# Performance work log

Hardware: AMD Instinct MI355X
Metric: run time of the kernel (lower is better)

## Reference

```python
import jax, jax.numpy as jnp
import numpy as np

B, T, D, H, K, V = 2, 2048, 2048, 16, 128, 128


def _l2norm(x, eps=1e-12):
    # F.normalize(p=2, dim=-1)
    n = jnp.sqrt(jnp.sum(x * x, axis=-1, keepdims=True))
    return x / jnp.maximum(n, eps)


def setup_inputs() -> dict:
    key = jax.random.key(0)
    ks = jax.random.split(key, 7)
    s = D ** -0.5
    return {
        "x": jax.random.normal(ks[0], (B, T, D), jnp.float32),
        "Wq": jax.random.normal(ks[1], (H * K, D), jnp.float32) * s,
        "Wk": jax.random.normal(ks[2], (H * K, D), jnp.float32) * s,
        "Wv": jax.random.normal(ks[3], (H * V, D), jnp.float32) * s,
        "Wa": jax.random.normal(ks[4], (H, D), jnp.float32) * s,
        "ba": jnp.zeros((H,), jnp.float32),
        "Wb": jax.random.normal(ks[5], (H, D), jnp.float32) * s,
        "bb": jnp.zeros((H,), jnp.float32),
    }


def _forward(x, Wq, Wk, Wv, Wa, ba, Wb, bb):
    Bq, Tq, _ = x.shape
    # projections (nn.Linear: y = x @ W.T)
    q = _l2norm(jnp.einsum('btd,od->bto', x, Wq).reshape(Bq, Tq, H, K))
    k = _l2norm(jnp.einsum('btd,od->bto', x, Wk).reshape(Bq, Tq, H, K))
    v = jnp.einsum('btd,od->bto', x, Wv).reshape(Bq, Tq, H, V)
    alpha = jax.nn.sigmoid(jnp.einsum('btd,hd->bth', x, Wa) + ba)          # [B,T,H] decay in (0,1)
    beta = jax.nn.softplus(jnp.einsum('btd,hd->bth', x, Wb) + bb) * K ** (-0.5)

    # gated delta rule recurrence over time (vectorized over B,H):
    #   S_t = a_t * S_{t-1} (I - b_t k_t k_t^T) + b_t v_t k_t^T ;  o_t = S_t q_t
    def step(S, inp):
        q_t, k_t, v_t, a_t, b_t = inp  # [B,H,K],[B,H,K],[B,H,V],[B,H],[B,H]
        Sd = S * a_t[..., None, None]                              # decay  [B,H,V,K]
        pred = jnp.einsum('bhvk,bhk->bhv', Sd, k_t)                # S k
        u = b_t[..., None] * (v_t - pred)                          # delta update [B,H,V]
        S_new = Sd + u[..., None] * k_t[:, :, None, :]             # rank-1 write
        o_t = jnp.einsum('bhvk,bhk->bhv', S_new, q_t)
        return S_new, o_t

    S0 = jnp.zeros((Bq, H, V, K), x.dtype)
    xs = (q.transpose(1, 0, 2, 3), k.transpose(1, 0, 2, 3),
          v.transpose(1, 0, 2, 3), alpha.transpose(1, 0, 2), beta.transpose(1, 0, 2))
    _, o = jax.lax.scan(step, S0, xs)
    return o.transpose(1, 0, 2, 3)  # [B,T,H,V]


def reference(x, Wq, Wk, Wv, Wa, ba, Wb, bb):
    return _forward(x, Wq, Wk, Wv, Wa, ba, Wb, bb)
```

## Files before the change

kernel.cpp:

```cpp
#include <hip/hip_runtime.h>
#include <math.h>

#define BB 2
#define TT 2048
#define DD 2048
#define HH 16
#define KK 128

typedef _Float16 h4 __attribute__((ext_vector_type(4)));
typedef _Float16 v8h __attribute__((ext_vector_type(8)));
typedef float v4f __attribute__((ext_vector_type(4)));
typedef float f2 __attribute__((ext_vector_type(2)));
typedef unsigned int u2v __attribute__((ext_vector_type(2)));

__global__ __launch_bounds__(256) void gemm_nt3(const float* __restrict__ A,
                                                const float* __restrict__ W0,
                                                const float* __restrict__ W1,
                                                const float* __restrict__ W2,
                                                float* __restrict__ Cbase,
                                                int M, int N, int Kd) {
  __shared__ float As[8][128];
  __shared__ float Bs[8][128];
  const int z = blockIdx.z;
  const float* W = (z == 0) ? W0 : (z == 1) ? W1 : W2;
  float* C = Cbase + (size_t)z * M * N;
  const int tid = threadIdx.x;
  const int bm = blockIdx.y * 128;
  const int bn = blockIdx.x * 128;
  const int lrow = tid >> 1;
  const int lcol = (tid & 1) * 4;
  const int rm = (tid >> 4) * 8;
  const int rn = (tid & 15) * 8;
  const float* Ap = A + (size_t)(bm + lrow) * Kd + lcol;
  const float* Wp = W + (size_t)(bn + lrow) * Kd + lcol;
  float acc[8][8];
#pragma unroll
  for (int i = 0; i < 8; i++)
#pragma unroll
    for (int j = 0; j < 8; j++) acc[i][j] = 0.f;
  float4 av = *(const float4*)Ap;
  float4 wv = *(const float4*)Wp;
  for (int d0 = 0; d0 < Kd; d0 += 8) {
    __syncthreads();
    As[lcol + 0][lrow] = av.x; As[lcol + 1][lrow] = av.y;
    As[lcol + 2][lrow] = av.z; As[lcol + 3][lrow] = av.w;
    Bs[lcol + 0][lrow] = wv.x; Bs[lcol + 1][lrow] = wv.y;
    Bs[lcol + 2][lrow] = wv.z; Bs[lcol + 3][lrow] = wv.w;
    __syncthreads();
    if (d0 + 8 < Kd) {
      av = *(const float4*)(Ap + d0 + 8);
      wv = *(const float4*)(Wp + d0 + 8);
    }
#pragma unroll
    for (int kk = 0; kk < 8; kk++) {
      const float4 a0 = *(const float4*)&As[kk][rm];
      const float4 a1 = *(const float4*)&As[kk][rm + 4];
      const float4 b0 = *(const float4*)&Bs[kk][rn];
      const float4 b1 = *(const float4*)&Bs[kk][rn + 4];
      const float ar[8] = {a0.x, a0.y, a0.z, a0.w, a1.x, a1.y, a1.z, a1.w};
      const float br[8] = {b0.x, b0.y, b0.z, b0.w, b1.x, b1.y, b1.z, b1.w};
#pragma unroll
      for (int i = 0; i < 8; i++)
#pragma unroll
        for (int j = 0; j < 8; j++) acc[i][j] = fmaf(ar[i], br[j], acc[i][j]);
    }
  }
#pragma unroll
  for (int i = 0; i < 8; i++) {
    float* cp = C + (size_t)(bm + rm + i) * N + bn + rn;
    float4 c0 = {acc[i][0], acc[i][1], acc[i][2], acc[i][3]};
    float4 c1 = {acc[i][4], acc[i][5], acc[i][6], acc[i][7]};
    *(float4*)cp = c0;
    *(float4*)(cp + 4) = c1;
  }
}

__global__ __launch_bounds__(256) void convert_f16(
    const float* __restrict__ x, const float* __restrict__ Wq,
    const float* __restrict__ Wk, const float* __restrict__ Wv,
    _Float16* __restrict__ xh, _Float16* __restrict__ Wf) {
  const size_t N4X = (size_t)BB * TT * DD / 4;
  const size_t N4W = (size_t)(HH * KK) * DD / 4;
  const size_t i = (size_t)blockIdx.x * 256 + threadIdx.x;
  if (i < N4X) {
    const float4 v = ((const float4*)x)[i];
    h4 hi;
    hi.x = (_Float16)v.x; hi.y = (_Float16)v.y;
    hi.z = (_Float16)v.z; hi.w = (_Float16)v.w;
    ((h4*)xh)[i] = hi;
  } else {
    const size_t j = i - N4X;
    const float* Ws = (j < N4W) ? Wq : (j < 2 * N4W) ? Wk : Wv;
    const size_t jj = (j < N4W) ? j : (j < 2 * N4W) ? (j - N4W) : (j - 2 * N4W);
    const float4 v = ((const float4*)Ws)[jj];
    h4 hi;
    hi.x = (_Float16)v.x; hi.y = (_Float16)v.y;
    hi.z = (_Float16)v.z; hi.w = (_Float16)v.w;
    ((h4*)Wf)[j] = hi;
  }
}

#define GLDS(gp, lp)                                              \
  __builtin_amdgcn_global_load_lds(                               \
      (const __attribute__((address_space(1))) void*)(gp),        \
      (__attribute__((address_space(3))) void*)(lp), 16, 0, 0)

__global__ __launch_bounds__(256) void gemm_mfma(
    const _Float16* __restrict__ xh, const _Float16* __restrict__ Wf,
    float* __restrict__ Cbase) {
  __shared__ float4 lraw[1024];
  _Float16* Ah = (_Float16*)lraw;
  _Float16* Bs = Ah + 4096;

  const int z = blockIdx.z;
  const _Float16* W = Wf + (size_t)z * DD * (HH * KK);
  float* C = Cbase + (size_t)z * (BB * TT) * (HH * KK);

  const int tid = threadIdx.x;
  const int w = tid >> 6;
  const int lane = tid & 63;
  const int bm = blockIdx.y * 128;
  const int bn = blockIdx.x * 128;
  const int wm = (w & 1) * 64;
  const int wn = (w >> 1) * 64;
  const int m16 = lane & 15;
  const int quad = lane >> 4;

  const _Float16* gA = xh + (size_t)(bm + (tid >> 2)) * DD + (tid & 3) * 8;
  const _Float16* gB = W + (size_t)(bn + (tid >> 2)) * DD + (tid & 3) * 8;
  const int lb = w * 512;

  v4f acc[4][4];
#pragma unroll
  for (int i = 0; i < 4; i++)
#pragma unroll
    for (int j = 0; j < 4; j++) acc[i][j] = (v4f){0.f, 0.f, 0.f, 0.f};

  for (int d0 = 0; d0 < DD; d0 += 32) {
    GLDS(gA + d0, Ah + lb);
    GLDS(gA + d0 + 64 * DD, Ah + 2048 + lb);
    GLDS(gB + d0, Bs + lb);
    GLDS(gB + d0 + 64 * DD, Bs + 2048 + lb);
    __syncthreads();
    v8h ah[4], bw[4];
#pragma unroll
    for (int i = 0; i < 4; i++) {
      ah[i] = *(const v8h*)&Ah[(wm + i * 16 + m16) * 32 + quad * 8];
      bw[i] = *(const v8h*)&Bs[(wn + i * 16 + m16) * 32 + quad * 8];
    }
#pragma unroll
    for (int mi = 0; mi < 4; mi++)
#pragma unroll
      for (int ni = 0; ni < 4; ni++)
        acc[mi][ni] = __builtin_amdgcn_mfma_f32_16x16x32_f16(ah[mi], bw[ni],
                                                             acc[mi][ni], 0, 0, 0);
    __syncthreads();
  }
#pragma unroll
  for (int mi = 0; mi < 4; mi++) {
#pragma unroll
    for (int r = 0; r < 4; r++) {
      float* cp =
          C + (size_t)(bm + wm + mi * 16 + quad * 4 + r) * (HH * KK) + bn + wn + m16;
#pragma unroll
      for (int ni = 0; ni < 4; ni++) cp[ni * 16] = acc[mi][ni][r];
    }
  }
}

__global__ __launch_bounds__(256) void ab_proj(const float* __restrict__ x,
                                               const float* __restrict__ Wa,
                                               const float* __restrict__ ba,
                                               const float* __restrict__ Wb,
                                               const float* __restrict__ bb,
                                               float* __restrict__ abq) {
  const int row = blockIdx.x;
  const int g = threadIdx.x >> 6;
  const int lane = threadIdx.x & 63;
  const int h0 = (g & 1) * 8;
  const bool isA = (g < 2);
  const float* W = isA ? Wa : Wb;
  const float* xr = x + (size_t)row * DD;
  float acc[8];
#pragma unroll
  for (int j = 0; j < 8; j++) acc[j] = 0.f;
  for (int d = lane; d < DD; d += 64) {
    const float xv = xr[d];
#pragma unroll
    for (int j = 0; j < 8; j++)
      acc[j] = fmaf(xv, W[(size_t)(h0 + j) * DD + d], acc[j]);
  }
#pragma unroll
  for (int j = 0; j < 8; j++) {
#pragma unroll
    for (int off = 32; off > 0; off >>= 1) acc[j] += __shfl_xor(acc[j], off, 64);
  }
  if (lane == 0) {
    if (isA) {
#pragma unroll
      for (int j = 0; j < 8; j++) {
        const float z = acc[j] + ba[h0 + j];
        abq[((size_t)row * HH + h0 + j) * 4 + 0] = 1.0f / (1.0f + expf(-z));
      }
    } else {
#pragma unroll
      for (int j = 0; j < 8; j++) {
        const float z = acc[j] + bb[h0 + j];
        const float sp = (z > 20.f) ? z : log1pf(expf(z));
        abq[((size_t)row * HH + h0 + j) * 4 + 1] = sp * 0.08838834764831845f;
      }
    }
  }
}

__global__ __launch_bounds__(256) void norm_qk(float* __restrict__ q,
                                               float* __restrict__ k,
                                               float* __restrict__ abq) {
  const int vec = blockIdx.x * 4 + (threadIdx.x >> 6);
  const int l = threadIdx.x & 63;
  float* qp = q + (size_t)vec * 128;
  float* kp = k + (size_t)vec * 128;
  float q0 = qp[l], q1 = qp[l + 64];
  float k0 = kp[l], k1 = kp[l + 64];
  float sq = q0 * q0 + q1 * q1;
  float sk = k0 * k0 + k1 * k1;
#pragma unroll
  for (int off = 32; off > 0; off >>= 1) {
    sq += __shfl_xor(sq, off, 64);
    sk += __shfl_xor(sk, off, 64);
  }
  const float iq = 1.0f / fmaxf(sqrtf(sq), 1e-12f);
  const float ik = 1.0f / fmaxf(sqrtf(sk), 1e-12f);
  q0 *= iq; q1 *= iq; k0 *= ik; k1 *= ik;
  qp[l] = q0; qp[l + 64] = q1;
  kp[l] = k0; kp[l + 64] = k1;
  float pq = q0 * k0 + q1 * k1;
#pragma unroll
  for (int off = 32; off > 0; off >>= 1) pq += __shfl_xor(pq, off, 64);
  if (l == 0) {
    abq[(size_t)vec * 4 + 2] = pq;
    abq[(size_t)vec * 4 + 3] =
        abq[(size_t)vec * 4 + 0] * abq[(size_t)vec * 4 + 1];
  }
}

#define DPP_ADD(x, ctrl)                                                     \
  ((x) + __int_as_float(__builtin_amdgcn_update_dpp(                         \
             0, __float_as_int(x), (ctrl), 0xF, 0xF, true)))

__device__ __forceinline__ float xadd32(float x) {
  const u2v r = __builtin_amdgcn_permlane32_swap(__float_as_uint(x),
                                                 __float_as_uint(x), false,
                                                 false);
  return __uint_as_float(r.x) + __uint_as_float(r.y);
}

#define SBAR() asm volatile("s_barrier" ::: "memory")
#define WAITV(n) asm volatile("s_waitcnt vmcnt(" #n ")" ::: "memory")

#define SCAN_MATH(kc, qc, vc, ac, jj, obname)                                  \
  {                                                                            \
    const f2 ka = {kc.x, kc.y};                                                \
    const f2 kb2 = {kc.z, kc.w};                                               \
    const f2 qa = {qc.x, qc.y};                                                \
    const f2 qb2 = {qc.z, qc.w};                                               \
    const f2 pdk = __builtin_elementwise_fma(Sb, kb2, Sa * ka);                \
    const f2 pdq = __builtin_elementwise_fma(Sb, qb2, Sa * qa);                \
    float dk = pdk.x + pdk.y;                                                  \
    float dq = pdq.x + pdq.y;                                                  \
    dk = DPP_ADD(dk, 0xB1);  dq = DPP_ADD(dq, 0xB1);                           \
    dk = DPP_ADD(dk, 0x4E);  dq = DPP_ADD(dq, 0x4E);                           \
    dk = DPP_ADD(dk, 0x141); dq = DPP_ADD(dq, 0x141);                          \
    dk = DPP_ADD(dk, 0x140); dq = DPP_ADD(dq, 0x140);                          \
    dk = xadd32(dk);         dq = xadd32(dq);                                  \
    const float u = ac.y * fmaf(-ac.x, dk, vc);                                \
    const float oo = fmaf(ac.x, dq, u * ac.z);                                 \
    const f2 a2 = {ac.x, ac.x};                                                \
    const f2 u2 = {u, u};                                                      \
    Sa = __builtin_elementwise_fma(a2, Sa, u2 * ka);                           \
    Sb = __builtin_elementwise_fma(a2, Sb, u2 * kb2);                          \
    obname = (ks == (jj)) ? oo : obname;                                       \
  }

#define STAGE(bi, tg)                                                          \
  {                                                                            \
    const float* gk =                                                          \
        kU + (size_t)((tg) + 2 * w + (lane >> 5)) * 2048 + (lane & 31) * 4;    \
    GLDS(gk, &Kb[bi][2 * w][0]);                                               \
    const float* gq =                                                          \
        qU + (size_t)((tg) + 2 * w + (lane >> 5)) * 2048 + (lane & 31) * 4;    \
    GLDS(gq, &Qb[bi][2 * w][0]);                                               \
    if (lane < 8) GLDS(aU + (size_t)((tg) + lane) * 64, &Ab[bi][0][0]);        \
    _Pragma("unroll") for (int jj = 0; jj < 8; jj++)                           \
        vf##bi[jj] = vU[vrow + (size_t)((tg) + jj) * 2048];                    \
  }

#define COMPUTE_GROUP(bi, obname)                                              \
  float obname = 0.f;                                                          \
  _Pragma("unroll") for (int j = 0; j < 8; j++) {                              \
    const float4 kc = *(const float4*)&Kb[bi][j][ks4];                         \
    const float4 qc = *(const float4*)&Qb[bi][j][ks4];                         \
    const float4 ac = *(const float4*)&Ab[bi][j][0];                           \
    const float vc = vf##bi[j];                                                \
    SCAN_MATH(kc, qc, vc, ac, j, obname);                                      \
  }

__global__ __launch_bounds__(256, 2) void scan_kernel(
    const float* __restrict__ q, const float* __restrict__ k,
    const float* __restrict__ v, const float* __restrict__ abq,
    float* __restrict__ o) {
  __shared__ float Kb[2][8][128];
  __shared__ float Qb[2][8][128];
  __shared__ float Ab[2][8][4];

  const int bid = blockIdx.x;
  const int bh = bid & 31;
  const int s = bid >> 5;
  const int h = bh & 15;
  const int b = bh >> 4;
  const int tid = threadIdx.x;
  const int w = tid >> 6;
  const int lane = tid & 63;
  const int rg = (lane >> 4) & 1;
  const int ks = (lane & 15) | ((lane >> 5) << 4);
  const int ks4 = ks * 4;
  const int vrow = s * 8 + w * 2 + rg;

  const size_t base = (size_t)b * TT * 2048 + (size_t)h * KK;
  const float* kU = k + base;
  const float* qU = q + base;
  const float* vU = v + base;
  const float* aU = abq + ((size_t)b * TT * HH + h) * 4;
  float* oU = o + base;

  f2 Sa = {0.f, 0.f}, Sb = {0.f, 0.f};
  float vf0[8], vf1[8];

  STAGE(0, 0);
  STAGE(1, 8);
  WAITV(11);
  SBAR();
  __builtin_amdgcn_sched_barrier(0);

  int tg = 0;
  for (int gp = 0; gp < TT / 8; gp += 2) {
    COMPUTE_GROUP(0, ob0);
    if (ks < 8) oU[vrow + (size_t)(tg + ks) * 2048] = ob0;
    SBAR();
    if (gp + 2 < TT / 8) {
      STAGE(0, tg + 16);
      WAITV(11);
    } else {
      WAITV(0);
    }
    SBAR();
    __builtin_amdgcn_sched_barrier(0);

    COMPUTE_GROUP(1, ob1);
    if (ks < 8) oU[vrow + (size_t)(tg + 8 + ks) * 2048] = ob1;
    SBAR();
    if (gp + 3 < TT / 8) {
      STAGE(1, tg + 24);
      WAITV(11);
    } else {
      WAITV(0);
    }
    SBAR();
    __builtin_amdgcn_sched_barrier(0);

    tg += 16;
  }
}

__global__ __launch_bounds__(64) void chunk_prep(
    const float* __restrict__ q, const float* __restrict__ k,
    const float* __restrict__ v, const float* __restrict__ abq,
    float* __restrict__ cT2, float* __restrict__ cMq,
    float* __restrict__ cTbv, float* __restrict__ cgv,
    float* __restrict__ cwv, float* __restrict__ cgC) {
  __shared__ float Ks[32][132];
  __shared__ float Qs[32][132];
  __shared__ float G[32][33];
  __shared__ float Gq[32][33];
  __shared__ float Tm[32][33];
  __shared__ float la[32], lg[32], bs_[32];

  const int c = blockIdx.x;
  const int b = c >> 10, h = (c >> 6) & 15, ci = c & 63;
  const int l = threadIdx.x;
  const size_t rowbase = (size_t)b * TT + ci * 32;

#pragma unroll
  for (int seg = 0; seg < 16; ++seg) {
    const int idx = l + 64 * seg;
    const int r = idx >> 5, cq = (idx & 31) * 4;
    const size_t g = (rowbase + r) * 2048 + (size_t)h * KK + cq;
    *(float4*)&Ks[r][cq] = *(const float4*)&k[g];
    *(float4*)&Qs[r][cq] = *(const float4*)&q[g];
  }
  if (l < 32) {
    const size_t ar = ((rowbase + l) * HH + h) * 4;
    la[l] = log2f(abq[ar]);
    bs_[l] = abq[ar + 1];
  }
  __syncthreads();
  if (l < 32) {
    float s = 0.f;
    for (int r = 0; r <= l; ++r) s += la[r];
    lg[l] = s;
  }
  __syncthreads();
  const float lgC = lg[31];
  for (int p = l; p < 1024; p += 64) {
    const int s = p >> 5, r = p & 31;
    float aK = 0.f, aQ = 0.f;
#pragma unroll
    for (int kk2 = 0; kk2 < 128; kk2 += 4) {
      const float4 kr = *(const float4*)&Ks[r][kk2];
      const float4 ks2 = *(const float4*)&Ks[s][kk2];
      const float4 qs2 = *(const float4*)&Qs[s][kk2];
      aK = fmaf(kr.x, ks2.x, fmaf(kr.y, ks2.y, fmaf(kr.z, ks2.z, fmaf(kr.w, ks2.w, aK))));
      aQ = fmaf(kr.x, qs2.x, fmaf(kr.y, qs2.y, fmaf(kr.z, qs2.z, fmaf(kr.w, qs2.w, aQ))));
    }
    G[s][r] = aK;
    Gq[s][r] = aQ;
  }
  __syncthreads();
  for (int p = l; p < 1024; p += 64) {
    const int s = p >> 5, r = p & 31;
    const float ratio = exp2f(lg[s] - lg[r]);
    const float Lv = (r < s) ? bs_[s] * ratio * G[s][r] : 0.f;
    const float Mv = (r <= s) ? ratio * Gq[s][r] : 0.f;
    G[s][r] = Lv;
    cMq[(size_t)c * 1024 + s * 32 + r] = Mv;
  }
  __syncthreads();
  if (l < 32) {
    for (int s = 0; s < 32; ++s) {
      float acc = 0.f;
      for (int r = 0; r < s; ++r) acc = fmaf(G[s][r], Tm[r][l], acc);
      Tm[s][l] = ((l == s) ? 1.f : 0.f) - acc;
      asm volatile("s_waitcnt lgkmcnt(0)" ::: "memory");
    }
  }
  __syncthreads();
  for (int p = l; p < 1024; p += 64) {
    const int s = p >> 5, r = p & 31;
    cT2[(size_t)c * 1024 + s * 32 + r] = Tm[s][r] * (bs_[r] * exp2f(lg[r]));
  }
  if (l < 32) {
    cgv[(size_t)c * 32 + l] = exp2f(lg[l]);
    cwv[(size_t)c * 32 + l] = exp2f(lgC - lg[l]);
    if (l == 0) cgC[c] = exp2f(lgC);
  }
  __syncthreads();
#pragma unroll
  for (int seg = 0; seg < 16; ++seg) {
    const int idx = l + 64 * seg;
    const int r = idx >> 5, cq = (idx & 31) * 4;
    const size_t g = (rowbase + r) * 2048 + (size_t)h * KK + cq;
    float4 vv = *(const float4*)&v[g];
    const float br = bs_[r];
    vv.x *= br; vv.y *= br; vv.z *= br; vv.w *= br;
    *(float4*)&Ks[r][cq] = vv;
  }
  __syncthreads();
  if (l < 32) {
    for (int ib = 0; ib < 8; ++ib) {
      float4 a0 = {0, 0, 0, 0}, a1 = {0, 0, 0, 0};
      float4 a2 = {0, 0, 0, 0}, a3 = {0, 0, 0, 0};
      for (int r = 0; r < 32; ++r) {
        const float tmr = Tm[l][r];
        const float4 v0 = *(const float4*)&Ks[r][ib * 16 + 0];
        const float4 v1 = *(const float4*)&Ks[r][ib * 16 + 4];
        const float4 v2 = *(const float4*)&Ks[r][ib * 16 + 8];
        const float4 v3 = *(const float4*)&Ks[r][ib * 16 + 12];
        a0.x = fmaf(tmr, v0.x, a0.x); a0.y = fmaf(tmr, v0.y, a0.y);
        a0.z = fmaf(tmr, v0.z, a0.z); a0.w = fmaf(tmr, v0.w, a0.w);
        a1.x = fmaf(tmr, v1.x, a1.x); a1.y = fmaf(tmr, v1.y, a1.y);
        a1.z = fmaf(tmr, v1.z, a1.z); a1.w = fmaf(tmr, v1.w, a1.w);
        a2.x = fmaf(tmr, v2.x, a2.x); a2.y = fmaf(tmr, v2.y, a2.y);
        a2.z = fmaf(tmr, v2.z, a2.z); a2.w = fmaf(tmr, v2.w, a2.w);
        a3.x = fmaf(tmr, v3.x, a3.x); a3.y = fmaf(tmr, v3.y, a3.y);
        a3.z = fmaf(tmr, v3.z, a3.z); a3.w = fmaf(tmr, v3.w, a3.w);
      }
      float* dst = &cTbv[(size_t)c * 4096 + l * 128 + ib * 16];
      *(float4*)(dst + 0) = a0;
      *(float4*)(dst + 4) = a1;
      *(float4*)(dst + 8) = a2;
      *(float4*)(dst + 12) = a3;
    }
  }
}

__global__ __launch_bounds__(256) void chunk_scan(
    const float* __restrict__ q, const float* __restrict__ k,
    const float* __restrict__ cT2, const float* __restrict__ cMq,
    const float* __restrict__ cTbv, const float* __restrict__ cgv,
    const float* __restrict__ cwv, const float* __restrict__ cgC,
    float* __restrict__ o) {
  __shared__ float Ss[16][132];
  __shared__ float Ks[32][132];
  __shared__ float Qs[32][132];
  __shared__ float Ps[16][33];
  __shared__ float Pqs[16][33];
  __shared__ float Us[32][17];
  __shared__ float T2s[32][36];
  __shared__ float Mqs[32][36];
  __shared__ float Tbs[32][20];
  __shared__ float gv[32], wv[32];

  const int blk = blockIdx.x;
  const int head = blk >> 3, vb = blk & 7;
  const int b = head >> 4, h = head & 15;
  const int vb0 = vb * 16;
  const int t = threadIdx.x;

  for (int i = t; i < 16 * 132; i += 256) ((float*)Ss)[i] = 0.f;

  const int sU = t & 31, ipU = t >> 5;
  const int i0 = 2 * ipU, i1 = i0 + 1;
  const int iO = t & 15, tr0 = (t >> 4) * 2;
  const int iS = t >> 4, kb = (t & 15) * 8;

  for (int ci = 0; ci < 64; ++ci) {
    const int c = (head << 6) + ci;
    const size_t rowbase = (size_t)b * TT + ci * 32;
    __syncthreads();
#pragma unroll
    for (int seg = 0; seg < 4; ++seg) {
      const int idx = t + 256 * seg;
      const int r = idx >> 5, cq = (idx & 31) * 4;
      const size_t g = (rowbase + r) * 2048 + (size_t)h * KK + cq;
      *(float4*)&Ks[r][cq] = *(const float4*)&k[g];
      *(float4*)&Qs[r][cq] = *(const float4*)&q[g];
    }
    {
      const int r = t >> 3, cq = (t & 7) * 4;
      *(float4*)&T2s[r][cq] = *(const float4*)&cT2[(size_t)c * 1024 + r * 32 + cq];
      *(float4*)&Mqs[r][cq] = *(const float4*)&cMq[(size_t)c * 1024 + r * 32 + cq];
    }
    if (t < 128) {
      const int r = t >> 2, cq = (t & 3) * 4;
      *(float4*)&Tbs[r][cq] =
          *(const float4*)&cTbv[(size_t)c * 4096 + r * 128 + vb0 + cq];
    }
    if (t < 32) {
      gv[t] = cgv[(size_t)c * 32 + t];
      wv[t] = cwv[(size_t)c * 32 + t];
    }
    const float gc = cgC[c];
    __syncthreads();
    {
      float p0 = 0.f, p1 = 0.f, pq0 = 0.f, pq1 = 0.f;
#pragma unroll
      for (int kk2 = 0; kk2 < 128; kk2 += 4) {
        const float4 s0 = *(const float4*)&Ss[i0][kk2];
        const float4 s1 = *(const float4*)&Ss[i1][kk2];
        const float4 kv = *(const float4*)&Ks[sU][kk2];
        const float4 qv = *(const float4*)&Qs[sU][kk2];
        p0 = fmaf(s0.x, kv.x, fmaf(s0.y, kv.y, fmaf(s0.z, kv.z, fmaf(s0.w, kv.w, p0))));
        p1 = fmaf(s1.x, kv.x, fmaf(s1.y, kv.y, fmaf(s1.z, kv.z, fmaf(s1.w, kv.w, p1))));
        pq0 = fmaf(s0.x, qv.x, fmaf(s0.y, qv.y, fmaf(s0.z, qv.z, fmaf(s0.w, qv.w, pq0))));
        pq1 = fmaf(s1.x, qv.x, fmaf(s1.y, qv.y, fmaf(s1.z, qv.z, fmaf(s1.w, qv.w, pq1))));
      }
      Ps[i0][sU] = p0; Ps[i1][sU] = p1;
      Pqs[i0][sU] = pq0; Pqs[i1][sU] = pq1;
    }
    __syncthreads();
    {
      float u0 = Tbs[sU][i0], u1 = Tbs[sU][i1];
#pragma unroll
      for (int r = 0; r < 32; ++r) {
        const float t2 = T2s[sU][r];
        u0 = fmaf(-t2, Ps[i0][r], u0);
        u1 = fmaf(-t2, Ps[i1][r], u1);
      }
      Us[sU][i0] = u0; Us[sU][i1] = u1;
    }
    __syncthreads();
    {
      float o0 = gv[tr0] * Pqs[iO][tr0];
      float o1 = gv[tr0 + 1] * Pqs[iO][tr0 + 1];
#pragma unroll
      for (int s2 = 0; s2 < 32; ++s2) {
        const float uu = Us[s2][iO];
        o0 = fmaf(Mqs[tr0][s2], uu, o0);
        o1 = fmaf(Mqs[tr0 + 1][s2], uu, o1);
      }
      const size_t og = (rowbase + tr0) * 2048 + (size_t)h * KK + vb0 + iO;
      o[og] = o0;
      o[og + 2048] = o1;
    }
    {
      float acc[8];
#pragma unroll
      for (int j = 0; j < 8; ++j) acc[j] = gc * Ss[iS][kb + j];
#pragma unroll
      for (int s2 = 0; s2 < 32; ++s2) {
        const float cw = wv[s2] * Us[s2][iS];
        const float4 k0 = *(const float4*)&Ks[s2][kb];
        const float4 k1 = *(const float4*)&Ks[s2][kb + 4];
        acc[0] = fmaf(cw, k0.x, acc[0]); acc[1] = fmaf(cw, k0.y, acc[1]);
        acc[2] = fmaf(cw, k0.z, acc[2]); acc[3] = fmaf(cw, k0.w, acc[3]);
        acc[4] = fmaf(cw, k1.x, acc[4]); acc[5] = fmaf(cw, k1.y, acc[5]);
        acc[6] = fmaf(cw, k1.z, acc[6]); acc[7] = fmaf(cw, k1.w, acc[7]);
      }
#pragma unroll
      for (int j = 0; j < 8; ++j) Ss[iS][kb + j] = acc[j];
    }
  }
}

extern "C" void kernel_launch(void* const* d_in, const int* in_sizes, int n_in,
                              void* d_out, int out_size, void* d_ws,
                              size_t ws_size, hipStream_t stream) {
  const float* x = (const float*)d_in[0];
  const float* Wq = (const float*)d_in[1];
  const float* Wk = (const float*)d_in[2];
  const float* Wv = (const float*)d_in[3];
  const float* Wa = (const float*)d_in[4];
  const float* ba = (const float*)d_in[5];
  const float* Wb = (const float*)d_in[6];
  const float* bb = (const float*)d_in[7];
  float* out = (float*)d_out;
  float* ws = (float*)d_ws;

  const size_t PROJ = (size_t)BB * TT * HH * KK;
  const size_t NABQ = (size_t)BB * TT * HH * 4;
  float* qw = ws;
  float* kw = ws + PROJ;
  float* vw = ws + 2 * PROJ;
  float* abq = ws + 3 * PROJ;
  _Float16* xh = (_Float16*)(abq + NABQ);
  _Float16* Wf = xh + (size_t)BB * TT * DD;
  float* cT2 = (float*)(Wf + 3 * (size_t)(HH * KK) * DD);
  float* cMq = cT2 + (size_t)2048 * 1024;
  float* cTbv = cMq + (size_t)2048 * 1024;
  float* cgv = cTbv + (size_t)2048 * 4096;
  float* cwv = cgv + (size_t)2048 * 32;
  float* cgC = cwv + (size_t)2048 * 32;

  const size_t NEED = (3 * PROJ + NABQ) * 4 +
                      ((size_t)BB * TT * DD + 3 * (size_t)(HH * KK) * DD) * 2;
  const size_t NEED2 =
      NEED + ((size_t)2048 * 1024 * 2 + (size_t)2048 * 4096 + 2048 * 64 + 2048) * 4;

  const int M = BB * TT;
  const int N = HH * KK;
  if (ws_size >= NEED) {
    const int cgrid = (int)(((size_t)BB * TT * DD / 4 + 3 * (size_t)N * DD / 4) / 256);
    convert_f16<<<cgrid, 256, 0, stream>>>(x, Wq, Wk, Wv, xh, Wf);
    gemm_mfma<<<dim3(N / 128, M / 128, 3), 256, 0, stream>>>(xh, Wf, qw);
  } else {
    gemm_nt3<<<dim3(N / 128, M / 128, 3), 256, 0, stream>>>(x, Wq, Wk, Wv, qw,
                                                            M, N, DD);
  }
  ab_proj<<<M, 256, 0, stream>>>(x, Wa, ba, Wb, bb, abq);
  norm_qk<<<(BB * TT * HH) / 4, 256, 0, stream>>>(qw, kw, abq);
  if (ws_size >= NEED2) {
    chunk_prep<<<2048, 64, 0, stream>>>(qw, kw, vw, abq, cT2, cMq, cTbv, cgv,
                                        cwv, cgC);
    chunk_scan<<<256, 256, 0, stream>>>(qw, kw, cT2, cMq, cTbv, cgv, cwv, cgC,
                                        out);
  } else {
    scan_kernel<<<BB * HH * 16, 256, 0, stream>>>(qw, kw, vw, abq, out);
  }
}
```

Measured before the change: 860.0 us.

## Split chunk scan into more blocks and widen chunk_prep to 256 threads

After: 982.0 us. +14.2%, slower.

```diff
diff --git a/kernel.cpp b/kernel.cpp
--- a/kernel.cpp
+++ b/kernel.cpp
@@ -372,14 +372,14 @@
   }
 }
 
-__global__ __launch_bounds__(64) void chunk_prep(
+__global__ __launch_bounds__(256) void chunk_prep(
     const float* __restrict__ q, const float* __restrict__ k,
     const float* __restrict__ v, const float* __restrict__ abq,
     float* __restrict__ cT2, float* __restrict__ cMq,
     float* __restrict__ cTbv, float* __restrict__ cgv,
     float* __restrict__ cwv, float* __restrict__ cgC) {
-  __shared__ float Ks[32][132];
-  __shared__ float Qs[32][132];
+  __shared__ float Ks[32][133];
+  __shared__ float Qs[32][133];
   __shared__ float G[32][33];
   __shared__ float Gq[32][33];
   __shared__ float Tm[32][33];
@@ -387,31 +387,31 @@
 
   const int c = blockIdx.x;
   const int b = c >> 10, h = (c >> 6) & 15, ci = c & 63;
-  const int l = threadIdx.x;
+  const int t = threadIdx.x;
   const size_t rowbase = (size_t)b * TT + ci * 32;
 
 #pragma unroll
-  for (int seg = 0; seg < 16; ++seg) {
-    const int idx = l + 64 * seg;
+  for (int seg = 0; seg < 4; ++seg) {
+    const int idx = t + 256 * seg;
     const int r = idx >> 5, cq = (idx & 31) * 4;
     const size_t g = (rowbase + r) * 2048 + (size_t)h * KK + cq;
     *(float4*)&Ks[r][cq] = *(const float4*)&k[g];
     *(float4*)&Qs[r][cq] = *(const float4*)&q[g];
   }
-  if (l < 32) {
-    const size_t ar = ((rowbase + l) * HH + h) * 4;
-    la[l] = log2f(abq[ar]);
-    bs_[l] = abq[ar + 1];
+  if (t < 32) {
+    const size_t ar = ((rowbase + t) * HH + h) * 4;
+    la[t] = log2f(abq[ar]);
+    bs_[t] = abq[ar + 1];
   }
   __syncthreads();
-  if (l < 32) {
+  if (t < 32) {
     float s = 0.f;
-    for (int r = 0; r <= l; ++r) s += la[r];
-    lg[l] = s;
+    for (int r = 0; r <= t; ++r) s += la[r];
+    lg[t] = s;
   }
   __syncthreads();
   const float lgC = lg[31];
-  for (int p = l; p < 1024; p += 64) {
+  for (int p = t; p < 1024; p += 256) {
     const int s = p >> 5, r = p & 31;
     float aK = 0.f, aQ = 0.f;
 #pragma unroll
@@ -426,7 +426,7 @@
     Gq[s][r] = aQ;
   }
   __syncthreads();
-  for (int p = l; p < 1024; p += 64) {
+  for (int p = t; p < 1024; p += 256) {
     const int s = p >> 5, r = p & 31;
     const float ratio = exp2f(lg[s] - lg[r]);
     const float Lv = (r < s) ? bs_[s] * ratio * G[s][r] : 0.f;
@@ -435,28 +435,28 @@
     cMq[(size_t)c * 1024 + s * 32 + r] = Mv;
   }
   __syncthreads();
-  if (l < 32) {
+  if (t < 32) {
     for (int s = 0; s < 32; ++s) {
       float acc = 0.f;
-      for (int r = 0; r < s; ++r) acc = fmaf(G[s][r], Tm[r][l], acc);
-      Tm[s][l] = ((l == s) ? 1.f : 0.f) - acc;
+      for (int r = 0; r < s; ++r) acc = fmaf(G[s][r], Tm[r][t], acc);
+      Tm[s][t] = ((t == s) ? 1.f : 0.f) - acc;
       asm volatile("s_waitcnt lgkmcnt(0)" ::: "memory");
     }
   }
   __syncthreads();
-  for (int p = l; p < 1024; p += 64) {
+  for (int p = t; p < 1024; p += 256) {
     const int s = p >> 5, r = p & 31;
     cT2[(size_t)c * 1024 + s * 32 + r] = Tm[s][r] * (bs_[r] * exp2f(lg[r]));
   }
-  if (l < 32) {
-    cgv[(size_t)c * 32 + l] = exp2f(lg[l]);
-    cwv[(size_t)c * 32 + l] = exp2f(lgC - lg[l]);
-    if (l == 0) cgC[c] = exp2f(lgC);
+  if (t < 32) {
+    cgv[(size_t)c * 32 + t] = exp2f(lg[t]);
+    cwv[(size_t)c * 32 + t] = exp2f(lgC - lg[t]);
+    if (t == 0) cgC[c] = exp2f(lgC);
   }
   __syncthreads();
 #pragma unroll
-  for (int seg = 0; seg < 16; ++seg) {
-    const int idx = l + 64 * seg;
+  for (int seg = 0; seg < 4; ++seg) {
+    const int idx = t + 256 * seg;
     const int r = idx >> 5, cq = (idx & 31) * 4;
     const size_t g = (rowbase + r) * 2048 + (size_t)h * KK + cq;
     float4 vv = *(const float4*)&v[g];
@@ -465,63 +465,61 @@
     *(float4*)&Ks[r][cq] = vv;
   }
   __syncthreads();
-  if (l < 32) {
-    for (int ib = 0; ib < 8; ++ib) {
-      float4 a0 = {0, 0, 0, 0}, a1 = {0, 0, 0, 0};
-      float4 a2 = {0, 0, 0, 0}, a3 = {0, 0, 0, 0};
-      for (int r = 0; r < 32; ++r) {
-        const float tmr = Tm[l][r];
-        const float4 v0 = *(const float4*)&Ks[r][ib * 16 + 0];
-        const float4 v1 = *(const float4*)&Ks[r][ib * 16 + 4];
-        const float4 v2 = *(const float4*)&Ks[r][ib * 16 + 8];
-        const float4 v3 = *(const float4*)&Ks[r][ib * 16 + 12];
-        a0.x = fmaf(tmr, v0.x, a0.x); a0.y = fmaf(tmr, v0.y, a0.y);
-        a0.z = fmaf(tmr, v0.z, a0.z); a0.w = fmaf(tmr, v0.w, a0.w);
-        a1.x = fmaf(tmr, v1.x, a1.x); a1.y = fmaf(tmr, v1.y, a1.y);
-        a1.z = fmaf(tmr, v1.z, a1.z); a1.w = fmaf(tmr, v1.w, a1.w);
-        a2.x = fmaf(tmr, v2.x, a2.x); a2.y = fmaf(tmr, v2.y, a2.y);
-        a2.z = fmaf(tmr, v2.z, a2.z); a2.w = fmaf(tmr, v2.w, a2.w);
-        a3.x = fmaf(tmr, v3.x, a3.x); a3.y = fmaf(tmr, v3.y, a3.y);
-        a3.z = fmaf(tmr, v3.z, a3.z); a3.w = fmaf(tmr, v3.w, a3.w);
-      }
-      float* dst = &cTbv[(size_t)c * 4096 + l * 128 + ib * 16];
-      *(float4*)(dst + 0) = a0;
-      *(float4*)(dst + 4) = a1;
-      *(float4*)(dst + 8) = a2;
-      *(float4*)(dst + 12) = a3;
-    }
-  }
-}
-
-__global__ __launch_bounds__(256) void chunk_scan(
+  {
+    const int l = t >> 3, ib = t & 7;
+    float4 a0 = {0, 0, 0, 0}, a1 = {0, 0, 0, 0};
+    float4 a2 = {0, 0, 0, 0}, a3 = {0, 0, 0, 0};
+    for (int r = 0; r < 32; ++r) {
+      const float tmr = Tm[l][r];
+      const float4 v0 = *(const float4*)&Ks[r][ib * 16 + 0];
+      const float4 v1 = *(const float4*)&Ks[r][ib * 16 + 4];
+      const float4 v2 = *(const float4*)&Ks[r][ib * 16 + 8];
+      const float4 v3 = *(const float4*)&Ks[r][ib * 16 + 12];
+      a0.x = fmaf(tmr, v0.x, a0.x); a0.y = fmaf(tmr, v0.y, a0.y);
+      a0.z = fmaf(tmr, v0.z, a0.z); a0.w = fmaf(tmr, v0.w, a0.w);
+      a1.x = fmaf(tmr, v1.x, a1.x); a1.y = fmaf(tmr, v1.y, a1.y);
+      a1.z = fmaf(tmr, v1.z, a1.z); a1.w = fmaf(tmr, v1.w, a1.w);
+      a2.x = fmaf(tmr, v2.x, a2.x); a2.y = fmaf(tmr, v2.y, a2.y);
+      a2.z = fmaf(tmr, v2.z, a2.z); a2.w = fmaf(tmr, v2.w, a2.w);
+      a3.x = fmaf(tmr, v3.x, a3.x); a3.y = fmaf(tmr, v3.y, a3.y);
+      a3.z = fmaf(tmr, v3.z, a3.z); a3.w = fmaf(tmr, v3.w, a3.w);
+    }
+    float* dst = &cTbv[(size_t)c * 4096 + l * 128 + ib * 16];
+    *(float4*)(dst + 0) = a0;
+    *(float4*)(dst + 4) = a1;
+    *(float4*)(dst + 8) = a2;
+    *(float4*)(dst + 12) = a3;
+  }
+}
+
+__global__ __launch_bounds__(256, 2) void chunk_scan(
     const float* __restrict__ q, const float* __restrict__ k,
     const float* __restrict__ cT2, const float* __restrict__ cMq,
     const float* __restrict__ cTbv, const float* __restrict__ cgv,
     const float* __restrict__ cwv, const float* __restrict__ cgC,
     float* __restrict__ o) {
-  __shared__ float Ss[16][132];
-  __shared__ float Ks[32][132];
-  __shared__ float Qs[32][132];
-  __shared__ float Ps[16][33];
-  __shared__ float Pqs[16][33];
-  __shared__ float Us[32][17];
-  __shared__ float T2s[32][36];
-  __shared__ float Mqs[32][36];
-  __shared__ float Tbs[32][20];
+  __shared__ float Ss[8][133];
+  __shared__ float Ks[32][133];
+  __shared__ float Qs[32][133];
+  __shared__ float Ps[8][33];
+  __shared__ float Pqs[8][33];
+  __shared__ float Us[32][9];
+  __shared__ float T2s[32][37];
+  __shared__ float Mqs[32][37];
+  __shared__ float Tbs[32][9];
   __shared__ float gv[32], wv[32];
 
   const int blk = blockIdx.x;
-  const int head = blk >> 3, vb = blk & 7;
+  const int head = blk & 31, vb = blk >> 5;
   const int b = head >> 4, h = head & 15;
-  const int vb0 = vb * 16;
+  const int vb0 = vb * 8;
   const int t = threadIdx.x;
 
-  for (int i = t; i < 16 * 132; i += 256) ((float*)Ss)[i] = 0.f;
-
-  const int sU = t & 31, ipU = t >> 5;
-  const int i0 = 2 * ipU, i1 = i0 + 1;
-  const int iO = t & 15, tr0 = (t >> 4) * 2;
-  const int iS = t >> 4, kb = (t & 15) * 8;
+  for (int i = t; i < 8 * 133; i += 256) ((float*)Ss)[i] = 0.f;
+
+  const int sU = t & 31, iU = t >> 5;
+  const int rowO = t >> 3, cO = t & 7;
+  const int iS = t >> 5, kb = (t & 31) * 4;
 
   for (int ci = 0; ci < 64; ++ci) {
     const int c = (head << 6) + ci;
@@ -539,11 +537,7 @@
       const int r = t >> 3, cq = (t & 7) * 4;
       *(float4*)&T2s[r][cq] = *(const float4*)&cT2[(size_t)c * 1024 + r * 32 + cq];
       *(float4*)&Mqs[r][cq] = *(const float4*)&cMq[(size_t)c * 1024 + r * 32 + cq];
-    }
-    if (t < 128) {
-      const int r = t >> 2, cq = (t & 3) * 4;
-      *(float4*)&Tbs[r][cq] =
-          *(const float4*)&cTbv[(size_t)c * 4096 + r * 128 + vb0 + cq];
+      Tbs[r][t & 7] = cTbv[(size_t)c * 4096 + r * 128 + vb0 + (t & 7)];
     }
     if (t < 32) {
       gv[t] = cgv[(size_t)c * 32 + t];
@@ -552,62 +546,48 @@
     const float gc = cgC[c];
     __syncthreads();
     {
-      float p0 = 0.f, p1 = 0.f, pq0 = 0.f, pq1 = 0.f;
+      float p0 = 0.f, pq0 = 0.f;
 #pragma unroll
       for (int kk2 = 0; kk2 < 128; kk2 += 4) {
-        const float4 s0 = *(const float4*)&Ss[i0][kk2];
-        const float4 s1 = *(const float4*)&Ss[i1][kk2];
+        const float4 s0 = *(const float4*)&Ss[iU][kk2];
         const float4 kv = *(const float4*)&Ks[sU][kk2];
         const float4 qv = *(const float4*)&Qs[sU][kk2];
         p0 = fmaf(s0.x, kv.x, fmaf(s0.y, kv.y, fmaf(s0.z, kv.z, fmaf(s0.w, kv.w, p0))));
-        p1 = fmaf(s1.x, kv.x, fmaf(s1.y, kv.y, fmaf(s1.z, kv.z, fmaf(s1.w, kv.w, p1))));
         pq0 = fmaf(s0.x, qv.x, fmaf(s0.y, qv.y, fmaf(s0.z, qv.z, fmaf(s0.w, qv.w, pq0))));
-        pq1 = fmaf(s1.x, qv.x, fmaf(s1.y, qv.y, fmaf(s1.z, qv.z, fmaf(s1.w, qv.w, pq1))));
       }
-      Ps[i0][sU] = p0; Ps[i1][sU] = p1;
-      Pqs[i0][sU] = pq0; Pqs[i1][sU] = pq1;
+      Ps[iU][sU] = p0;
+      Pqs[iU][sU] = pq0;
     }
     __syncthreads();
     {
-      float u0 = Tbs[sU][i0], u1 = Tbs[sU][i1];
-#pragma unroll
-      for (int r = 0; r < 32; ++r) {
-        const float t2 = T2s[sU][r];
-        u0 = fmaf(-t2, Ps[i0][r], u0);
-        u1 = fmaf(-t2, Ps[i1][r], u1);
-      }
-      Us[sU][i0] = u0; Us[sU][i1] = u1;
+      float u0 = Tbs[sU][iU];
+#pragma unroll
+      for (int r = 0; r < 32; ++r) u0 = fmaf(-T2s[sU][r], Ps[iU][r], u0);
+      Us[sU][iU] = u0;
     }
     __syncthreads();
     {
-      float o0 = gv[tr0] * Pqs[iO][tr0];
-      float o1 = gv[tr0 + 1] * Pqs[iO][tr0 + 1];
-#pragma unroll
-      for (int s2 = 0; s2 < 32; ++s2) {
-        const float uu = Us[s2][iO];
-        o0 = fmaf(Mqs[tr0][s2], uu, o0);
-        o1 = fmaf(Mqs[tr0 + 1][s2], uu, o1);
-      }
-      const size_t og = (rowbase + tr0) * 2048 + (size_t)h * KK + vb0 + iO;
-      o[og] = o0;
-      o[og + 2048] = o1;
+      float o0 = gv[rowO] * Pqs[cO][rowO];
+#pragma unroll
+      for (int s2 = 0; s2 < 32; ++s2)
+        o0 = fmaf(Mqs[rowO][s2], Us[s2][cO], o0);
+      o[(rowbase + rowO) * 2048 + (size_t)h * KK + vb0 + cO] = o0;
     }
     {
-      float acc[8];
-#pragma unroll
-      for (int j = 0; j < 8; ++j) acc[j] = gc * Ss[iS][kb + j];
+      float acc0[4];
+#pragma unroll
+      for (int j = 0; j < 4; ++j) acc0[j] = gc * Ss[iS][kb + j];
 #pragma unroll
       for (int s2 = 0; s2 < 32; ++s2) {
         const float cw = wv[s2] * Us[s2][iS];
         const float4 k0 = *(const float4*)&Ks[s2][kb];
-        const float4 k1 = *(const float4*)&Ks[s2][kb + 4];
-        acc[0] = fmaf(cw, k0.x, acc[0]); acc[1] = fmaf(cw, k0.y, acc[1]);
-        acc[2] = fmaf(cw, k0.z, acc[2]); acc[3] = fmaf(cw, k0.w, acc[3]);
-        acc[4] = fmaf(cw, k1.x, acc[4]); acc[5] = fmaf(cw, k1.y, acc[5]);
-        acc[6] = fmaf(cw, k1.z, acc[6]); acc[7] = fmaf(cw, k1.w, acc[7]);
+        acc0[0] = fmaf(cw, k0.x, acc0[0]);
+        acc0[1] = fmaf(cw, k0.y, acc0[1]);
+        acc0[2] = fmaf(cw, k0.z, acc0[2]);
+        acc0[3] = fmaf(cw, k0.w, acc0[3]);
       }
 #pragma unroll
-      for (int j = 0; j < 8; ++j) Ss[iS][kb + j] = acc[j];
+      for (int j = 0; j < 4; ++j) Ss[iS][kb + j] = acc0[j];
     }
   }
 }
@@ -659,9 +639,9 @@
   ab_proj<<<M, 256, 0, stream>>>(x, Wa, ba, Wb, bb, abq);
   norm_qk<<<(BB * TT * HH) / 4, 256, 0, stream>>>(qw, kw, abq);
   if (ws_size >= NEED2) {
-    chunk_prep<<<2048, 64, 0, stream>>>(qw, kw, vw, abq, cT2, cMq, cTbv, cgv,
-                                        cwv, cgC);
-    chunk_scan<<<256, 256, 0, stream>>>(qw, kw, cT2, cMq, cTbv, cgv, cwv, cgC,
+    chunk_prep<<<2048, 256, 0, stream>>>(qw, kw, vw, abq, cT2, cMq, cTbv, cgv,
+                                         cwv, cgC);
+    chunk_scan<<<512, 256, 0, stream>>>(qw, kw, cT2, cMq, cTbv, cgv, cwv, cgC,
                                         out);
   } else {
     scan_kernel<<<BB * HH * 16, 256, 0, stream>>>(qw, kw, vw, abq, out);
```
